# Optimization experiments

Measured on AMD Instinct MI355X. Metric: run time of the kernel, lower is better.

The kernel has to match this reference:

```python
import jax, jax.numpy as jnp
import numpy as np

B, P, H, D = 16, 2048, 2048, 1024


def _length_mask(key, batch, seqlen):
    # random valid lengths in [seqlen//2, seqlen], mask[b, t] = 1.0 if t < len[b]
    lens = jax.random.randint(key, (batch,), seqlen // 2, seqlen + 1)
    return (jnp.arange(seqlen)[None, :] < lens[:, None]).astype(jnp.float32)


def setup_inputs() -> dict:
    key = jax.random.key(0)
    k1, k2, k3, k4 = jax.random.split(key, 4)
    return {
        "premise_batch": jax.random.normal(k1, (B, P, D), dtype=jnp.float32),
        "premise_mask": _length_mask(k2, B, P),
        "hypothesis_batch": jax.random.normal(k3, (B, H, D), dtype=jnp.float32),
        "hypothesis_mask": _length_mask(k4, B, H),
    }


def reference(premise_batch, premise_mask, hypothesis_batch, hypothesis_mask):
    d = hypothesis_batch.shape[-1]
    # (B, P, H) scaled dot-product similarity; dropout p=0 -> identity (eval mode)
    sim = jnp.einsum("bpd,bhd->bph", premise_batch, hypothesis_batch) / jnp.sqrt(
        jnp.asarray(d, dtype=premise_batch.dtype)
    )
    # ESIM masked_softmax: softmax of mask-multiplied logits, re-mask, renormalize
    kmask = hypothesis_mask[:, None, :]  # (B, 1, H)
    attn = jax.nn.softmax(sim * kmask, axis=-1)
    attn = attn * kmask
    attn = attn / (jnp.sum(attn, axis=-1, keepdims=True) + 1e-13)
    # ESIM weighted_sum: weighted sum of hypothesis vectors, zero padded premise rows
    out = jnp.einsum("bph,bhd->bpd", attn, hypothesis_batch)
    return out * premise_mask[:, :, None]
```

## Files before the change

kernel.cpp:

```cpp
#include <hip/hip_runtime.h>
#include <math.h>

typedef _Float16 f16;
typedef _Float16 f16x8 __attribute__((ext_vector_type(8)));
typedef _Float16 f16x4 __attribute__((ext_vector_type(4)));
typedef float    f32x4 __attribute__((ext_vector_type(4)));

#define NB 16
#define NP 2048
#define NH 2048
#define ND 1024
#define MT 32
#define NT 64
#define SCALE 0.03125f

__global__ __launch_bounds__(256)
void prep(const float* __restrict__ KV, f16* __restrict__ KVh, f16* __restrict__ KVt)
{
  __shared__ f16 tile[64][68];
  const int bb = blockIdx.z;
  const int h0 = blockIdx.y << 6;
  const int d0 = blockIdx.x << 6;
  const int tid = threadIdx.x;
  const int r0 = tid >> 4;
  const int c0 = (tid & 15) << 2;
#pragma unroll
  for (int i = 0; i < 4; ++i) {
    const int r = r0 + (i << 4);
    f32x4 v = *(const f32x4*)(KV + ((size_t)(bb * NH + h0 + r)) * ND + d0 + c0);
    f16x4 hv;
    hv[0] = (f16)v[0]; hv[1] = (f16)v[1]; hv[2] = (f16)v[2]; hv[3] = (f16)v[3];
    *(f16x4*)(KVh + ((size_t)(bb * NH + h0 + r)) * ND + d0 + c0) = hv;
    *(f16x4*)&tile[r][c0] = hv;
  }
  __syncthreads();
#pragma unroll
  for (int i = 0; i < 4; ++i) {
    const int dr = r0 + (i << 4);
    f16x4 hv;
#pragma unroll
    for (int j = 0; j < 4; ++j) hv[j] = tile[c0 + j][dr];
    *(f16x4*)(KVt + ((size_t)(bb * ND + d0 + dr)) * NH + h0 + c0) = hv;
  }
}

__global__ __launch_bounds__(256, 2)
void uniattn(const float* __restrict__ Q,   const float* __restrict__ PM,
             const f16*   __restrict__ KVh, const f16*   __restrict__ KVt,
             const float* __restrict__ HM,  float* __restrict__ OUT)
{
  const int bid  = blockIdx.x;
  const int b    = bid >> 6;
  const int p0   = (bid & 63) * MT;
  const int tid  = threadIdx.x;
  const int w    = tid >> 6;
  const int lane = tid & 63;
  const int qd   = lane >> 4;
  const int c16  = lane & 15;
  const int rt   = w & 1;
  const int wp   = w >> 1;

  if (PM[(size_t)b * NP + p0] == 0.0f) {
    float* ob = OUT + ((size_t)b * NP + p0) * ND;
    const f32x4 z = {0.f, 0.f, 0.f, 0.f};
#pragma unroll
    for (int i = 0; i < 32; ++i)
      *(f32x4*)(ob + (size_t)((i << 8) + tid) * 4) = z;
    return;
  }

  __shared__ f16 Qs[32 * 1024];
  __shared__ float pm_s[2][2][16];
  __shared__ float pl_s[2][2][16];
  __shared__ float m_s[32];
  __shared__ float l_s[32];
  __shared__ float a_s[32];
  __shared__ float rec_s[32];
  __shared__ int   nt_s;
  __shared__ __align__(16) f16 Pt[32][72];

  const float* hm = HM + (size_t)b * NH;

  {
    const float* Qb = Q + ((size_t)b * NP + p0) * ND;
#pragma unroll
    for (int i = 0; i < 16; ++i) {
      const int g = (i << 8) + tid;
      const int r = g >> 7;
      const int c = g & 127;
      f32x4 x = *(const f32x4*)(Qb + (size_t)r * ND + (c << 3));
      f32x4 y = *(const f32x4*)(Qb + (size_t)r * ND + (c << 3) + 4);
      f16x8 hv;
      hv[0] = (f16)(x[0] * SCALE); hv[1] = (f16)(x[1] * SCALE);
      hv[2] = (f16)(x[2] * SCALE); hv[3] = (f16)(x[3] * SCALE);
      hv[4] = (f16)(y[0] * SCALE); hv[5] = (f16)(y[1] * SCALE);
      hv[6] = (f16)(y[2] * SCALE); hv[7] = (f16)(y[3] * SCALE);
      *(f16x8*)&Qs[(r << 10) + ((c ^ (r & 7)) << 3)] = hv;
    }
  }
  if (tid < 32) { m_s[tid] = -1e30f; l_s[tid] = 0.0f; }
  if (w == 0) {
    const int idx = (lane < 32) ? (lane << 6) : 0;
    unsigned long long bal = __ballot(hm[idx] != 0.0f);
    if (lane == 0) nt_s = __popcll(bal) - 32;
  }
  __syncthreads();
  const int ntiles = nt_s;

  f32x4 Oacc[2][16];
#pragma unroll
  for (int r2 = 0; r2 < 2; ++r2)
#pragma unroll
    for (int t = 0; t < 16; ++t)
      Oacc[r2][t] = (f32x4){0.f, 0.f, 0.f, 0.f};

  const f16* Kb = KVh + (size_t)b * NH * ND;
  const f16* Vt = KVt + (size_t)b * ND * NH;
  const int dbase = w << 8;
  const int ar = rt * 16 + c16;
  const int rx = ar & 7;

#pragma unroll 1
  for (int it = 0; it < ntiles; ++it) {
    const int h0 = it << 6;
    f32x4 S0 = {0.f,0.f,0.f,0.f}, S1 = {0.f,0.f,0.f,0.f};
    const f16* kr0 = Kb + (size_t)(h0 + wp * 32 + c16) * ND + (qd << 3);
    const f16* kr1 = kr0 + (size_t)16 * ND;
#pragma unroll 4
    for (int kc = 0; kc < 32; ++kc) {
      f16x8 af = *(const f16x8*)&Qs[(ar << 10) + ((((kc << 2) + qd) ^ rx) << 3)];
      f16x8 b0 = *(const f16x8*)(kr0 + (kc << 5));
      f16x8 b1 = *(const f16x8*)(kr1 + (kc << 5));
      S0 = __builtin_amdgcn_mfma_f32_16x16x32_f16(af, b0, S0, 0, 0, 0);
      S1 = __builtin_amdgcn_mfma_f32_16x16x32_f16(af, b1, S1, 0, 0, 0);
    }

    const float km0 = hm[h0 + wp * 32 + c16];
    const float km1 = hm[h0 + wp * 32 + 16 + c16];
    float sm0[4], sm1[4], mx[4];
#pragma unroll
    for (int rg = 0; rg < 4; ++rg) {
      sm0[rg] = (km0 != 0.f) ? S0[rg] : -1e30f;
      sm1[rg] = (km1 != 0.f) ? S1[rg] : -1e30f;
      mx[rg] = fmaxf(sm0[rg], sm1[rg]);
    }
#pragma unroll
    for (int sh = 1; sh < 16; sh <<= 1)
#pragma unroll
      for (int rg = 0; rg < 4; ++rg)
        mx[rg] = fmaxf(mx[rg], __shfl_xor(mx[rg], sh));
    if (c16 == 0) {
#pragma unroll
      for (int rg = 0; rg < 4; ++rg) pm_s[rt][wp][qd*4+rg] = mx[rg];
    }
    __syncthreads();
    if (wp == 0 && c16 == 0) {
#pragma unroll
      for (int rg = 0; rg < 4; ++rg) {
        const int rr = qd*4+rg, r = rt*16+rr;
        const float mt = fmaxf(pm_s[rt][0][rr], pm_s[rt][1][rr]);
        const float mo = m_s[r];
        const float mn = fmaxf(mo, mt);
        a_s[r] = __expf(mo - mn);
        m_s[r] = mn;
      }
    }
    __syncthreads();

    float ls[4] = {0.f,0.f,0.f,0.f};
#pragma unroll
    for (int rg = 0; rg < 4; ++rg) {
      const int row = rt*16 + qd*4 + rg;
      const float mn = m_s[row];
      const float pv0 = km0 * __expf(sm0[rg] - mn);
      const float pv1 = km1 * __expf(sm1[rg] - mn);
      Pt[row][wp*32 + c16]      = (f16)pv0;
      Pt[row][wp*32 + 16 + c16] = (f16)pv1;
      ls[rg] = pv0 + pv1;
    }
#pragma unroll
    for (int sh = 1; sh < 16; sh <<= 1)
#pragma unroll
      for (int rg = 0; rg < 4; ++rg)
        ls[rg] += __shfl_xor(ls[rg], sh);
    if (c16 == 0) {
#pragma unroll
      for (int rg = 0; rg < 4; ++rg) pl_s[rt][wp][qd*4+rg] = ls[rg];
    }
    __syncthreads();
    if (wp == 0 && c16 == 0) {
#pragma unroll
      for (int rg = 0; rg < 4; ++rg) {
        const int rr = qd*4+rg, r = rt*16+rr;
        l_s[r] = l_s[r] * a_s[r] + pl_s[rt][0][rr] + pl_s[rt][1][rr];
      }
    }

#pragma unroll
    for (int r2 = 0; r2 < 2; ++r2) {
      float av[4];
#pragma unroll
      for (int rg = 0; rg < 4; ++rg) av[rg] = a_s[r2*16 + qd*4 + rg];
#pragma unroll
      for (int t = 0; t < 16; ++t)
#pragma unroll
        for (int rg = 0; rg < 4; ++rg) Oacc[r2][t][rg] *= av[rg];
    }
#pragma unroll
    for (int kc2 = 0; kc2 < 2; ++kc2) {
      f16x8 pa0 = *(const f16x8*)&Pt[c16][kc2*32 + qd*8];
      f16x8 pa1 = *(const f16x8*)&Pt[16 + c16][kc2*32 + qd*8];
      const f16* vrow = Vt + (size_t)(dbase + c16) * NH + h0 + kc2*32 + (qd << 3);
#pragma unroll
      for (int t = 0; t < 16; ++t) {
        f16x8 vb = *(const f16x8*)(vrow + (size_t)t * 16 * NH);
        Oacc[0][t] = __builtin_amdgcn_mfma_f32_16x16x32_f16(pa0, vb, Oacc[0][t], 0, 0, 0);
        Oacc[1][t] = __builtin_amdgcn_mfma_f32_16x16x32_f16(pa1, vb, Oacc[1][t], 0, 0, 0);
      }
    }
    __syncthreads();
  }

  if (tid < 32) rec_s[tid] = PM[(size_t)b * NP + p0 + tid] / (l_s[tid] + 1e-13f);
  __syncthreads();
#pragma unroll
  for (int r2 = 0; r2 < 2; ++r2) {
    float rv[4];
#pragma unroll
    for (int rg = 0; rg < 4; ++rg) rv[rg] = rec_s[r2*16 + qd*4 + rg];
#pragma unroll
    for (int t = 0; t < 16; ++t) {
      float* op = OUT + ((size_t)b * NP + p0 + r2*16 + qd*4) * ND + (w << 8) + t*16 + c16;
#pragma unroll
      for (int rg = 0; rg < 4; ++rg)
        op[(size_t)rg * ND] = Oacc[r2][t][rg] * rv[rg];
    }
  }
}

extern "C" void kernel_launch(void* const* d_in, const int* in_sizes, int n_in,
                              void* d_out, int out_size, void* d_ws, size_t ws_size,
                              hipStream_t stream) {
  const float* Q  = (const float*)d_in[0];
  const float* PM = (const float*)d_in[1];
  const float* KV = (const float*)d_in[2];
  const float* HM = (const float*)d_in[3];
  float* OUT = (float*)d_out;

  f16* KVh = (f16*)d_ws;
  f16* KVt = KVh + (size_t)NB * NH * ND;
  (void)ws_size; (void)in_sizes; (void)n_in; (void)out_size;

  dim3 pgrid(ND / 64, NH / 64, NB);
  hipLaunchKernelGGL(prep, pgrid, dim3(256), 0, stream, KV, KVh, KVt);

  dim3 grid(NB * (NP / MT));
  hipLaunchKernelGGL(uniattn, grid, dim3(256), 0, stream, Q, PM, KVh, KVt, HM, OUT);
}
```

Measured before the change: 1.558 ms.

## Double-buffer K loads, batch V loads, raise MFMA priority and swizzle block order

Block IDs are remapped so that blocks of neighbouring batches interleave across the grid, which may help cache locality across XCDs. The QK^T loop now prefetches the next group of K fragments into alternating register buffers while the current group feeds the MFMAs. The PV loop issues all V loads for a half-tile before running its MFMAs. The MFMA sections are wrapped in s_setprio to favour matrix issue. The extra live registers risk spilling or lower occupancy under launch_bounds(256,2).

```diff
diff --git a/kernel.cpp b/kernel.cpp
--- a/kernel.cpp
+++ b/kernel.cpp
@@ -49,7 +49,8 @@
              const f16*   __restrict__ KVh, const f16*   __restrict__ KVt,
              const float* __restrict__ HM,  float* __restrict__ OUT)
 {
-  const int bid  = blockIdx.x;
+  const int orig = blockIdx.x;
+  const int bid  = ((orig & 7) << 7) + (orig >> 3);
   const int b    = bid >> 6;
   const int p0   = (bid & 63) * MT;
   const int tid  = threadIdx.x;
@@ -119,24 +120,47 @@
   const int dbase = w << 8;
   const int ar = rt * 16 + c16;
   const int rx = ar & 7;
+  const f16* krA = Kb + (size_t)(wp * 32 + c16) * ND + (qd << 3);
 
 #pragma unroll 1
   for (int it = 0; it < ntiles; ++it) {
     const int h0 = it << 6;
-    f32x4 S0 = {0.f,0.f,0.f,0.f}, S1 = {0.f,0.f,0.f,0.f};
-    const f16* kr0 = Kb + (size_t)(h0 + wp * 32 + c16) * ND + (qd << 3);
+    const f16* kr0 = krA + (size_t)h0 * ND;
     const f16* kr1 = kr0 + (size_t)16 * ND;
-#pragma unroll 4
-    for (int kc = 0; kc < 32; ++kc) {
-      f16x8 af = *(const f16x8*)&Qs[(ar << 10) + ((((kc << 2) + qd) ^ rx) << 3)];
-      f16x8 b0 = *(const f16x8*)(kr0 + (kc << 5));
-      f16x8 b1 = *(const f16x8*)(kr1 + (kc << 5));
-      S0 = __builtin_amdgcn_mfma_f32_16x16x32_f16(af, b0, S0, 0, 0, 0);
-      S1 = __builtin_amdgcn_mfma_f32_16x16x32_f16(af, b1, S1, 0, 0, 0);
-    }
-
     const float km0 = hm[h0 + wp * 32 + c16];
     const float km1 = hm[h0 + wp * 32 + 16 + c16];
+    f32x4 S0 = {0.f,0.f,0.f,0.f}, S1 = {0.f,0.f,0.f,0.f};
+    f16x8 ka0[4], kb0[4], ka1[4], kb1[4];
+#pragma unroll
+    for (int j = 0; j < 4; ++j) {
+      ka0[j] = *(const f16x8*)(kr0 + (j << 5));
+      kb0[j] = *(const f16x8*)(kr1 + (j << 5));
+    }
+#pragma unroll
+    for (int g = 0; g < 8; ++g) {
+      if (g < 7) {
+#pragma unroll
+        for (int j = 0; j < 4; ++j) {
+          const int kc = (g + 1) * 4 + j;
+          if (g & 1) { ka0[j] = *(const f16x8*)(kr0 + (kc << 5));
+                       kb0[j] = *(const f16x8*)(kr1 + (kc << 5)); }
+          else       { ka1[j] = *(const f16x8*)(kr0 + (kc << 5));
+                       kb1[j] = *(const f16x8*)(kr1 + (kc << 5)); }
+        }
+      }
+      __builtin_amdgcn_s_setprio(1);
+#pragma unroll
+      for (int j = 0; j < 4; ++j) {
+        const int kc = g * 4 + j;
+        f16x8 af = *(const f16x8*)&Qs[(ar << 10) + ((((kc << 2) + qd) ^ rx) << 3)];
+        f16x8 va = (g & 1) ? ka1[j] : ka0[j];
+        f16x8 vk = (g & 1) ? kb1[j] : kb0[j];
+        S0 = __builtin_amdgcn_mfma_f32_16x16x32_f16(af, va, S0, 0, 0, 0);
+        S1 = __builtin_amdgcn_mfma_f32_16x16x32_f16(af, vk, S1, 0, 0, 0);
+      }
+      __builtin_amdgcn_s_setprio(0);
+    }
+
     float sm0[4], sm1[4], mx[4];
 #pragma unroll
     for (int rg = 0; rg < 4; ++rg) {
@@ -206,17 +230,29 @@
 #pragma unroll
         for (int rg = 0; rg < 4; ++rg) Oacc[r2][t][rg] *= av[rg];
     }
-#pragma unroll
-    for (int kc2 = 0; kc2 < 2; ++kc2) {
-      f16x8 pa0 = *(const f16x8*)&Pt[c16][kc2*32 + qd*8];
-      f16x8 pa1 = *(const f16x8*)&Pt[16 + c16][kc2*32 + qd*8];
-      const f16* vrow = Vt + (size_t)(dbase + c16) * NH + h0 + kc2*32 + (qd << 3);
-#pragma unroll
-      for (int t = 0; t < 16; ++t) {
-        f16x8 vb = *(const f16x8*)(vrow + (size_t)t * 16 * NH);
-        Oacc[0][t] = __builtin_amdgcn_mfma_f32_16x16x32_f16(pa0, vb, Oacc[0][t], 0, 0, 0);
-        Oacc[1][t] = __builtin_amdgcn_mfma_f32_16x16x32_f16(pa1, vb, Oacc[1][t], 0, 0, 0);
-      }
+    const f16* vrow = Vt + (size_t)(dbase + c16) * NH + h0 + (qd << 3);
+#pragma unroll
+    for (int kcc = 0; kcc < 2; ++kcc) {
+      f16x8 pa0 = *(const f16x8*)&Pt[c16][kcc*32 + qd*8];
+      f16x8 pa1 = *(const f16x8*)&Pt[16 + c16][kcc*32 + qd*8];
+      const f16* vc = vrow + (kcc << 5);
+      f16x8 vb0[8], vb1[8];
+#pragma unroll
+      for (int j = 0; j < 8; ++j) vb0[j] = *(const f16x8*)(vc + (size_t)j * (16 * NH));
+#pragma unroll
+      for (int j = 0; j < 8; ++j) vb1[j] = *(const f16x8*)(vc + (size_t)(8 + j) * (16 * NH));
+      __builtin_amdgcn_s_setprio(1);
+#pragma unroll
+      for (int j = 0; j < 8; ++j) {
+        Oacc[0][j] = __builtin_amdgcn_mfma_f32_16x16x32_f16(pa0, vb0[j], Oacc[0][j], 0, 0, 0);
+        Oacc[1][j] = __builtin_amdgcn_mfma_f32_16x16x32_f16(pa1, vb0[j], Oacc[1][j], 0, 0, 0);
+      }
+#pragma unroll
+      for (int j = 0; j < 8; ++j) {
+        Oacc[0][8+j] = __builtin_amdgcn_mfma_f32_16x16x32_f16(pa0, vb1[j], Oacc[0][8+j], 0, 0, 0);
+        Oacc[1][8+j] = __builtin_amdgcn_mfma_f32_16x16x32_f16(pa1, vb1[j], Oacc[1][8+j], 0, 0, 0);
+      }
+      __builtin_amdgcn_s_setprio(0);
     }
     __syncthreads();
   }
```

Measured after the change: 1.779 ms. +14.2%, slower.

## Halve query tile, keep softmax state in registers, skip masked key prep

Applied to the files above, without the earlier changes.

Shrinks the per-block query tile from 32 to 16 rows so each wave computes one 16x16 score block. Running max and sum now live in per-thread registers, which removes one barrier and the single-thread shared-memory updates per key tile. Occupancy is raised to 3 blocks per CU, and blocks are remapped so neighbouring blocks come from different batches. The prep kernel skips fully masked key tiles and uses wider 8-element vectors. The trade-off is that each block gets half the K/V reuse, so K and V global reads roughly double.

```diff
diff --git a/kernel.cpp b/kernel.cpp
--- a/kernel.cpp
+++ b/kernel.cpp
@@ -10,81 +10,80 @@
 #define NP 2048
 #define NH 2048
 #define ND 1024
-#define MT 32
+#define MT 16
 #define NT 64
 #define SCALE 0.03125f
 
 __global__ __launch_bounds__(256)
-void prep(const float* __restrict__ KV, f16* __restrict__ KVh, f16* __restrict__ KVt)
+void prep(const float* __restrict__ KV, const float* __restrict__ HM,
+          f16* __restrict__ KVh, f16* __restrict__ KVt)
 {
   __shared__ f16 tile[64][68];
   const int bb = blockIdx.z;
   const int h0 = blockIdx.y << 6;
   const int d0 = blockIdx.x << 6;
+  if (HM[(size_t)bb * NH + h0] == 0.0f) return;
   const int tid = threadIdx.x;
-  const int r0 = tid >> 4;
-  const int c0 = (tid & 15) << 2;
-#pragma unroll
-  for (int i = 0; i < 4; ++i) {
-    const int r = r0 + (i << 4);
-    f32x4 v = *(const f32x4*)(KV + ((size_t)(bb * NH + h0 + r)) * ND + d0 + c0);
-    f16x4 hv;
-    hv[0] = (f16)v[0]; hv[1] = (f16)v[1]; hv[2] = (f16)v[2]; hv[3] = (f16)v[3];
-    *(f16x4*)(KVh + ((size_t)(bb * NH + h0 + r)) * ND + d0 + c0) = hv;
-    *(f16x4*)&tile[r][c0] = hv;
+  const int r0 = tid >> 3;
+  const int c0 = (tid & 7) << 3;
+#pragma unroll
+  for (int i = 0; i < 2; ++i) {
+    const int r = r0 + (i << 5);
+    f32x4 x = *(const f32x4*)(KV + ((size_t)(bb * NH + h0 + r)) * ND + d0 + c0);
+    f32x4 y = *(const f32x4*)(KV + ((size_t)(bb * NH + h0 + r)) * ND + d0 + c0 + 4);
+    f16x8 hv;
+    hv[0] = (f16)x[0]; hv[1] = (f16)x[1]; hv[2] = (f16)x[2]; hv[3] = (f16)x[3];
+    hv[4] = (f16)y[0]; hv[5] = (f16)y[1]; hv[6] = (f16)y[2]; hv[7] = (f16)y[3];
+    *(f16x8*)(KVh + ((size_t)(bb * NH + h0 + r)) * ND + d0 + c0) = hv;
+    *(f16x8*)&tile[r][c0] = hv;
   }
   __syncthreads();
 #pragma unroll
-  for (int i = 0; i < 4; ++i) {
-    const int dr = r0 + (i << 4);
-    f16x4 hv;
-#pragma unroll
-    for (int j = 0; j < 4; ++j) hv[j] = tile[c0 + j][dr];
-    *(f16x4*)(KVt + ((size_t)(bb * ND + d0 + dr)) * NH + h0 + c0) = hv;
+  for (int i = 0; i < 2; ++i) {
+    const int dr = r0 + (i << 5);
+    f16x8 hv;
+#pragma unroll
+    for (int j = 0; j < 8; ++j) hv[j] = tile[c0 + j][dr];
+    *(f16x8*)(KVt + ((size_t)(bb * ND + d0 + dr)) * NH + h0 + c0) = hv;
   }
 }
 
-__global__ __launch_bounds__(256, 2)
+__global__ __launch_bounds__(256, 3)
 void uniattn(const float* __restrict__ Q,   const float* __restrict__ PM,
              const f16*   __restrict__ KVh, const f16*   __restrict__ KVt,
              const float* __restrict__ HM,  float* __restrict__ OUT)
 {
-  const int bid  = blockIdx.x;
-  const int b    = bid >> 6;
-  const int p0   = (bid & 63) * MT;
+  const int orig = blockIdx.x;
+  const int bid  = ((orig & 7) << 8) + (orig >> 3);
+  const int b    = bid >> 7;
+  const int p0   = (bid & 127) * MT;
   const int tid  = threadIdx.x;
   const int w    = tid >> 6;
   const int lane = tid & 63;
   const int qd   = lane >> 4;
   const int c16  = lane & 15;
-  const int rt   = w & 1;
-  const int wp   = w >> 1;
 
   if (PM[(size_t)b * NP + p0] == 0.0f) {
     float* ob = OUT + ((size_t)b * NP + p0) * ND;
     const f32x4 z = {0.f, 0.f, 0.f, 0.f};
 #pragma unroll
-    for (int i = 0; i < 32; ++i)
+    for (int i = 0; i < 16; ++i)
       *(f32x4*)(ob + (size_t)((i << 8) + tid) * 4) = z;
     return;
   }
 
-  __shared__ f16 Qs[32 * 1024];
-  __shared__ float pm_s[2][2][16];
-  __shared__ float pl_s[2][2][16];
-  __shared__ float m_s[32];
-  __shared__ float l_s[32];
-  __shared__ float a_s[32];
-  __shared__ float rec_s[32];
+  __shared__ f16 Qs[16 * 1024];
+  __shared__ float pm_s[4][16];
+  __shared__ float pl_s[4][16];
   __shared__ int   nt_s;
-  __shared__ __align__(16) f16 Pt[32][72];
+  __shared__ __align__(16) f16 Pt[16][72];
 
   const float* hm = HM + (size_t)b * NH;
 
   {
     const float* Qb = Q + ((size_t)b * NP + p0) * ND;
 #pragma unroll
-    for (int i = 0; i < 16; ++i) {
+    for (int i = 0; i < 8; ++i) {
       const int g = (i << 8) + tid;
       const int r = g >> 7;
       const int c = g & 127;
@@ -98,7 +97,6 @@
       *(f16x8*)&Qs[(r << 10) + ((c ^ (r & 7)) << 3)] = hv;
     }
   }
-  if (tid < 32) { m_s[tid] = -1e30f; l_s[tid] = 0.0f; }
   if (w == 0) {
     const int idx = (lane < 32) ? (lane << 6) : 0;
     unsigned long long bal = __ballot(hm[idx] != 0.0f);
@@ -107,42 +105,38 @@
   __syncthreads();
   const int ntiles = nt_s;
 
-  f32x4 Oacc[2][16];
-#pragma unroll
-  for (int r2 = 0; r2 < 2; ++r2)
-#pragma unroll
-    for (int t = 0; t < 16; ++t)
-      Oacc[r2][t] = (f32x4){0.f, 0.f, 0.f, 0.f};
+  float mrun[4] = {-1e30f, -1e30f, -1e30f, -1e30f};
+  float lrun[4] = {0.f, 0.f, 0.f, 0.f};
+
+  f32x4 Oacc[16];
+#pragma unroll
+  for (int t = 0; t < 16; ++t) Oacc[t] = (f32x4){0.f, 0.f, 0.f, 0.f};
 
   const f16* Kb = KVh + (size_t)b * NH * ND;
   const f16* Vt = KVt + (size_t)b * ND * NH;
   const int dbase = w << 8;
-  const int ar = rt * 16 + c16;
-  const int rx = ar & 7;
+  const int sx = c16 & 7;
+  const f16* krA = Kb + (size_t)((w << 4) + c16) * ND + (qd << 3);
+  const f16* vrow = Vt + (size_t)(dbase + c16) * NH + (qd << 3);
 
 #pragma unroll 1
   for (int it = 0; it < ntiles; ++it) {
     const int h0 = it << 6;
-    f32x4 S0 = {0.f,0.f,0.f,0.f}, S1 = {0.f,0.f,0.f,0.f};
-    const f16* kr0 = Kb + (size_t)(h0 + wp * 32 + c16) * ND + (qd << 3);
-    const f16* kr1 = kr0 + (size_t)16 * ND;
-#pragma unroll 4
+    const f16* kr = krA + (size_t)h0 * ND;
+    const float km = hm[h0 + (w << 4) + c16];
+    f32x4 S = {0.f, 0.f, 0.f, 0.f};
+#pragma unroll
     for (int kc = 0; kc < 32; ++kc) {
-      f16x8 af = *(const f16x8*)&Qs[(ar << 10) + ((((kc << 2) + qd) ^ rx) << 3)];
-      f16x8 b0 = *(const f16x8*)(kr0 + (kc << 5));
-      f16x8 b1 = *(const f16x8*)(kr1 + (kc << 5));
-      S0 = __builtin_amdgcn_mfma_f32_16x16x32_f16(af, b0, S0, 0, 0, 0);
-      S1 = __builtin_amdgcn_mfma_f32_16x16x32_f16(af, b1, S1, 0, 0, 0);
-    }
-
-    const float km0 = hm[h0 + wp * 32 + c16];
-    const float km1 = hm[h0 + wp * 32 + 16 + c16];
-    float sm0[4], sm1[4], mx[4];
+      f16x8 af = *(const f16x8*)&Qs[(c16 << 10) + ((((kc << 2) + qd) ^ sx) << 3)];
+      f16x8 kb = *(const f16x8*)(kr + (kc << 5));
+      S = __builtin_amdgcn_mfma_f32_16x16x32_f16(af, kb, S, 0, 0, 0);
+    }
+
+    float sm[4], mx[4];
 #pragma unroll
     for (int rg = 0; rg < 4; ++rg) {
-      sm0[rg] = (km0 != 0.f) ? S0[rg] : -1e30f;
-      sm1[rg] = (km1 != 0.f) ? S1[rg] : -1e30f;
-      mx[rg] = fmaxf(sm0[rg], sm1[rg]);
+      sm[rg] = (km != 0.f) ? S[rg] : -1e30f;
+      mx[rg] = sm[rg];
     }
 #pragma unroll
     for (int sh = 1; sh < 16; sh <<= 1)
@@ -151,32 +145,22 @@
         mx[rg] = fmaxf(mx[rg], __shfl_xor(mx[rg], sh));
     if (c16 == 0) {
 #pragma unroll
-      for (int rg = 0; rg < 4; ++rg) pm_s[rt][wp][qd*4+rg] = mx[rg];
+      for (int rg = 0; rg < 4; ++rg) pm_s[w][qd * 4 + rg] = mx[rg];
     }
     __syncthreads();
-    if (wp == 0 && c16 == 0) {
-#pragma unroll
-      for (int rg = 0; rg < 4; ++rg) {
-        const int rr = qd*4+rg, r = rt*16+rr;
-        const float mt = fmaxf(pm_s[rt][0][rr], pm_s[rt][1][rr]);
-        const float mo = m_s[r];
-        const float mn = fmaxf(mo, mt);
-        a_s[r] = __expf(mo - mn);
-        m_s[r] = mn;
-      }
-    }
-    __syncthreads();
-
-    float ls[4] = {0.f,0.f,0.f,0.f};
+
+    float al[4], ls[4];
 #pragma unroll
     for (int rg = 0; rg < 4; ++rg) {
-      const int row = rt*16 + qd*4 + rg;
-      const float mn = m_s[row];
-      const float pv0 = km0 * __expf(sm0[rg] - mn);
-      const float pv1 = km1 * __expf(sm1[rg] - mn);
-      Pt[row][wp*32 + c16]      = (f16)pv0;
-      Pt[row][wp*32 + 16 + c16] = (f16)pv1;
-      ls[rg] = pv0 + pv1;
+      const int row = qd * 4 + rg;
+      const float mt = fmaxf(fmaxf(pm_s[0][row], pm_s[1][row]),
+                             fmaxf(pm_s[2][row], pm_s[3][row]));
+      const float mn = fmaxf(mrun[rg], mt);
+      al[rg]   = __expf(mrun[rg] - mn);
+      mrun[rg] = mn;
+      const float pv = km * __expf(sm[rg] - mn);
+      Pt[row][(w << 4) + c16] = (f16)pv;
+      ls[rg] = pv;
     }
 #pragma unroll
     for (int sh = 1; sh < 16; sh <<= 1)
@@ -185,55 +169,41 @@
         ls[rg] += __shfl_xor(ls[rg], sh);
     if (c16 == 0) {
 #pragma unroll
-      for (int rg = 0; rg < 4; ++rg) pl_s[rt][wp][qd*4+rg] = ls[rg];
+      for (int rg = 0; rg < 4; ++rg) pl_s[w][qd * 4 + rg] = ls[rg];
     }
     __syncthreads();
-    if (wp == 0 && c16 == 0) {
-#pragma unroll
-      for (int rg = 0; rg < 4; ++rg) {
-        const int rr = qd*4+rg, r = rt*16+rr;
-        l_s[r] = l_s[r] * a_s[r] + pl_s[rt][0][rr] + pl_s[rt][1][rr];
+
+#pragma unroll
+    for (int rg = 0; rg < 4; ++rg) {
+      const int row = qd * 4 + rg;
+      lrun[rg] = lrun[rg] * al[rg] +
+                 (pl_s[0][row] + pl_s[1][row]) + (pl_s[2][row] + pl_s[3][row]);
+    }
+
+#pragma unroll
+    for (int t = 0; t < 16; ++t)
+#pragma unroll
+      for (int rg = 0; rg < 4; ++rg) Oacc[t][rg] *= al[rg];
+    const f16* vc = vrow + h0;
+#pragma unroll
+    for (int kcc = 0; kcc < 2; ++kcc) {
+      f16x8 pa = *(const f16x8*)&Pt[c16][kcc * 32 + (qd << 3)];
+#pragma unroll
+      for (int t = 0; t < 16; ++t) {
+        f16x8 vb = *(const f16x8*)(vc + (kcc << 5) + (size_t)t * (16 * NH));
+        Oacc[t] = __builtin_amdgcn_mfma_f32_16x16x32_f16(pa, vb, Oacc[t], 0, 0, 0);
       }
     }
-
-#pragma unroll
-    for (int r2 = 0; r2 < 2; ++r2) {
-      float av[4];
-#pragma unroll
-      for (int rg = 0; rg < 4; ++rg) av[rg] = a_s[r2*16 + qd*4 + rg];
-#pragma unroll
-      for (int t = 0; t < 16; ++t)
-#pragma unroll
-        for (int rg = 0; rg < 4; ++rg) Oacc[r2][t][rg] *= av[rg];
-    }
-#pragma unroll
-    for (int kc2 = 0; kc2 < 2; ++kc2) {
-      f16x8 pa0 = *(const f16x8*)&Pt[c16][kc2*32 + qd*8];
-      f16x8 pa1 = *(const f16x8*)&Pt[16 + c16][kc2*32 + qd*8];
-      const f16* vrow = Vt + (size_t)(dbase + c16) * NH + h0 + kc2*32 + (qd << 3);
-#pragma unroll
-      for (int t = 0; t < 16; ++t) {
-        f16x8 vb = *(const f16x8*)(vrow + (size_t)t * 16 * NH);
-        Oacc[0][t] = __builtin_amdgcn_mfma_f32_16x16x32_f16(pa0, vb, Oacc[0][t], 0, 0, 0);
-        Oacc[1][t] = __builtin_amdgcn_mfma_f32_16x16x32_f16(pa1, vb, Oacc[1][t], 0, 0, 0);
-      }
-    }
-    __syncthreads();
-  }
-
-  if (tid < 32) rec_s[tid] = PM[(size_t)b * NP + p0 + tid] / (l_s[tid] + 1e-13f);
-  __syncthreads();
-#pragma unroll
-  for (int r2 = 0; r2 < 2; ++r2) {
-    float rv[4];
-#pragma unroll
-    for (int rg = 0; rg < 4; ++rg) rv[rg] = rec_s[r2*16 + qd*4 + rg];
+  }
+
+#pragma unroll
+  for (int rg = 0; rg < 4; ++rg) {
+    const float rv = PM[(size_t)b * NP + p0 + qd * 4 + rg] / (lrun[rg] + 1e-13f);
 #pragma unroll
     for (int t = 0; t < 16; ++t) {
-      float* op = OUT + ((size_t)b * NP + p0 + r2*16 + qd*4) * ND + (w << 8) + t*16 + c16;
-#pragma unroll
-      for (int rg = 0; rg < 4; ++rg)
-        op[(size_t)rg * ND] = Oacc[r2][t][rg] * rv[rg];
+      float* op = OUT + ((size_t)b * NP + p0 + qd * 4 + rg) * ND
+                      + dbase + t * 16 + c16;
+      *op = Oacc[t][rg] * rv;
     }
   }
 }
@@ -252,7 +222,7 @@
   (void)ws_size; (void)in_sizes; (void)n_in; (void)out_size;
 
   dim3 pgrid(ND / 64, NH / 64, NB);
-  hipLaunchKernelGGL(prep, pgrid, dim3(256), 0, stream, KV, KVh, KVt);
+  hipLaunchKernelGGL(prep, pgrid, dim3(256), 0, stream, KV, HM, KVh, KVt);
 
   dim3 grid(NB * (NP / MT));
   hipLaunchKernelGGL(uniattn, grid, dim3(256), 0, stream, Q, PM, KVh, KVt, HM, OUT);
```

Result: slower. 2.233 ms (+43.3%).
